# Kernel optimization log

Measured on AMD Instinct MI355X. Metric: run time of the kernel, lower is better.

Reference implementation:

```python
import jax, jax.numpy as jnp
import numpy as np

B, L, E, H, D = 32, 512, 256, 8, 64
SCALE = int(D ** 0.5)  # matches TF: int(hidden_dim ** 0.5) == 8


def setup_inputs() -> dict:
    key = jax.random.key(0)
    ks = jax.random.split(key, 6)
    return {
        "x": jax.random.normal(ks[0], (B, L, E), dtype=jnp.float32),
        "positional": jax.random.normal(ks[1], (L, E), dtype=jnp.float32) * 0.02,
        "Wq": jax.random.normal(ks[2], (H, E, D), dtype=jnp.float32) * 0.05,
        "Wk": jax.random.normal(ks[3], (H, E, D), dtype=jnp.float32) * 0.05,
        "Wv": jax.random.normal(ks[4], (H, E, D), dtype=jnp.float32) * 0.05,
        "Wo": jax.random.normal(ks[5], (H * D, E), dtype=jnp.float32) * 0.05,
    }


def reference(x, positional, Wq, Wk, Wv, Wo):
    act = jnp.tanh  # activation='tanh'
    xp = x + positional                                   # [B,L,E]
    # Batched per-head projections with activation applied post-matmul
    q = act(jnp.einsum('ble,hed->bhld', xp, Wq))          # [B,H,L,D]
    k = act(jnp.einsum('ble,hed->bhld', xp, Wk))
    v = act(jnp.einsum('ble,hed->bhld', xp, Wv))
    score = jnp.einsum('bhqd,bhkd->bhqk', q, k) / SCALE   # [B,H,L,L]
    attn = jax.nn.softmax(score, axis=-1)
    out = jnp.einsum('bhqk,bhkd->bhqd', attn, v)          # [B,H,L,D]
    # concat heads along last axis (head-major) -> [B,L,H*D]
    out = jnp.transpose(out, (0, 2, 1, 3)).reshape(B, L, H * D)
    return jnp.einsum('blf,fe->ble', out, Wo) + act(xp)   # [B,L,E]
```

## Files before the change

### kernel.cpp

```cpp
#include <hip/hip_runtime.h>
#include <cstdint>

#define NB 32
#define NL 512
#define NE 256
#define NH 8
#define ND 64
#define NM 16384
#define NHD 512

using half8  = __attribute__((ext_vector_type(8))) _Float16;
using half4  = __attribute__((ext_vector_type(4))) _Float16;
using f32x4  = __attribute__((ext_vector_type(4))) float;
using f32x16 = __attribute__((ext_vector_type(16))) float;
using u32x2  = __attribute__((ext_vector_type(2))) unsigned int;

__device__ __forceinline__ f32x4 mfma16(half8 a, half8 b, f32x4 c) {
    return __builtin_amdgcn_mfma_f32_16x16x32_f16(a, b, c, 0, 0, 0);
}
__device__ __forceinline__ f32x16 mfma32(half8 a, half8 b, f32x16 c) {
    return __builtin_amdgcn_mfma_f32_32x32x16_f16(a, b, c, 0, 0, 0);
}
__device__ __forceinline__ void cp16_g2l(const void* g, void* l) {
    __builtin_amdgcn_global_load_lds(
        (const __attribute__((address_space(1))) void*)g,
        (__attribute__((address_space(3))) void*)l, 16, 0, 0);
}
__device__ __forceinline__ float exp2fast(float x) {
    return __builtin_amdgcn_exp2f(x);
}
__device__ __forceinline__ float fast_tanh(float x) {
    float xc = fminf(fmaxf(x, -9.f), 9.f);
    float t = exp2fast(xc * 2.88539008178f);
    return (t - 1.f) * __builtin_amdgcn_rcpf(t + 1.f);
}
__device__ __forceinline__ uint32_t pk16(float a, float b) {
    auto h2 = __builtin_amdgcn_cvt_pkrtz(a, b);
    return __builtin_bit_cast(uint32_t, h2);
}

__global__ __launch_bounds__(256) void prep(
        const float* __restrict__ x, const float* __restrict__ pos,
        const float* __restrict__ Wq, const float* __restrict__ Wk,
        const float* __restrict__ Wv, const float* __restrict__ Wo,
        _Float16* __restrict__ wqkv, _Float16* __restrict__ woh,
        _Float16* __restrict__ xph) {
    int bid = blockIdx.x;
    if (bid < 2048) {
        int idx = bid * 256 + threadIdx.x;
        if (idx < 1536 * 256) {
            int n = idx >> 8, e = idx & 255;
            int s = n >> 9, h = (n >> 6) & 7, d = n & 63;
            const float* W = (s == 0) ? Wq : (s == 1) ? Wk : Wv;
            wqkv[idx] = (_Float16)W[(h * NE + e) * ND + d];
        } else {
            int j = idx - 1536 * 256;
            int e = j >> 9, f = j & 511;
            woh[j] = (_Float16)Wo[f * NE + e];
        }
    } else {
        int i = ((bid - 2048) * 256 + threadIdx.x) * 4;
        float4 xv = *(const float4*)(x + i);
        float4 pv = *(const float4*)(pos + (i & (NL * NE - 1)));
        half4 o;
        o[0] = (_Float16)(xv.x + pv.x);
        o[1] = (_Float16)(xv.y + pv.y);
        o[2] = (_Float16)(xv.z + pv.z);
        o[3] = (_Float16)(xv.w + pv.w);
        *(half4*)(xph + i) = o;
    }
}

__global__ __launch_bounds__(256) void proj_gemm(
        const _Float16* __restrict__ wqkv, const _Float16* __restrict__ xph,
        _Float16* __restrict__ q_all, _Float16* __restrict__ k_all,
        _Float16* __restrict__ vT) {
    __shared__ _Float16 Alds[128 * 64];
    __shared__ _Float16 Blds[128 * 64];
    int tid = threadIdx.x;
    int w = tid >> 6, l = tid & 63;
    int bid = blockIdx.x;
    int xcd = bid & 7, local = bid >> 3;
    int tn = local % 12;
    int tm = xcd * 16 + local / 12;
    int wn = w >> 1, wm = w & 1;
    int m16 = l & 15, g = l >> 4;
    bool isv = (tn >= 8);
    int lrow8 = l >> 3;
    int kc16 = (l & 7) ^ lrow8;
    f32x4 acc[4][4] = {};

    const _Float16* Ag = wqkv + (size_t)tn * 128 * 256;
    const _Float16* Bg = xph + (size_t)tm * 128 * 256;

    for (int kt = 0; kt < 4; ++kt) {
#pragma unroll
        for (int i = 0; i < 4; ++i) {
            int cA = w * 4 + i;
            int row = cA * 8 + lrow8;
            cp16_g2l(Ag + (size_t)row * 256 + kt * 64 + kc16 * 8,
                     Alds + cA * 512);
            cp16_g2l(Bg + (size_t)row * 256 + kt * 64 + kc16 * 8,
                     Blds + cA * 512);
        }
        __syncthreads();
#pragma unroll
        for (int ks = 0; ks < 2; ++ks) {
            half8 af[4], bf[4];
#pragma unroll
            for (int f = 0; f < 4; ++f) {
                int ra = wn * 64 + f * 16 + m16;
                int rb = wm * 64 + f * 16 + m16;
                af[f] = *(const half8*)(Alds + ra * 64 + (((ks * 4 + g) ^ (ra & 7)) << 3));
                bf[f] = *(const half8*)(Blds + rb * 64 + (((ks * 4 + g) ^ (rb & 7)) << 3));
            }
            if (!isv) {
#pragma unroll
                for (int nf = 0; nf < 4; ++nf)
#pragma unroll
                    for (int mf = 0; mf < 4; ++mf)
                        acc[nf][mf] = mfma16(af[nf], bf[mf], acc[nf][mf]);
            } else {
#pragma unroll
                for (int nf = 0; nf < 4; ++nf)
#pragma unroll
                    for (int mf = 0; mf < 4; ++mf)
                        acc[nf][mf] = mfma16(bf[mf], af[nf], acc[nf][mf]);
            }
        }
        __syncthreads();
    }
    if (!isv) {
        _Float16* dst = (tn < 4) ? q_all : k_all;
#pragma unroll
        for (int nf = 0; nf < 4; ++nf) {
            int c = (tn & 3) * 128 + wn * 64 + nf * 16 + g * 4;
#pragma unroll
            for (int mf = 0; mf < 4; ++mf) {
                int m = tm * 128 + wm * 64 + mf * 16 + m16;
                f32x4 v = acc[nf][mf];
                half4 hv;
#pragma unroll
                for (int r = 0; r < 4; ++r) hv[r] = (_Float16)fast_tanh(v[r]);
                *(half4*)(dst + (size_t)m * NHD + c) = hv;
            }
        }
    } else {
#pragma unroll
        for (int nf = 0; nf < 4; ++nf) {
            int c = (tn - 8) * 128 + wn * 64 + nf * 16 + m16;
#pragma unroll
            for (int mf = 0; mf < 4; ++mf) {
                int t0 = tm * 128 + wm * 64 + mf * 16 + g * 4;
                f32x4 v = acc[nf][mf];
                half4 hv;
#pragma unroll
                for (int r = 0; r < 4; ++r) hv[r] = (_Float16)fast_tanh(v[r]);
                *(half4*)(vT + (size_t)c * NM + t0) = hv;
            }
        }
    }
}

__global__ __launch_bounds__(256, 3) void attn_kernel(
        const _Float16* __restrict__ q_all, const _Float16* __restrict__ k_all,
        const _Float16* __restrict__ vT, _Float16* __restrict__ attn_out) {
    __shared__ _Float16 Klds[2][64 * 64];
    __shared__ _Float16 Vtlds[2][64 * 64];
    int tid = threadIdx.x;
    int w = tid >> 6, l = tid & 63;
    int l31 = l & 31, hi = l >> 5;
    int bid = blockIdx.x;
    int qt = bid & 3, h = (bid >> 2) & 7, b = bid >> 5;
    const float C1 = 0.125f * 1.44269504089f;

    int qbase = qt * 128 + w * 32;
    half8 qf[4];
    {
        const _Float16* qp = q_all + (size_t)(b * NL + qbase + l31) * NHD + h * ND + hi * 8;
#pragma unroll
        for (int ks = 0; ks < 4; ++ks) qf[ks] = *(const half8*)(qp + ks * 16);
    }

    f32x16 acc_o[2] = {};
    float mrow = -1e30f, lrow = 0.f;

    int st_row = tid >> 2;
    int st_u0 = (tid & 3) * 2;
    const _Float16* kg = k_all + (size_t)(b * NL + st_row) * NHD + h * ND + st_u0 * 8;
    const _Float16* vg = vT + (size_t)(h * ND + st_row) * NM + b * NL + st_u0 * 8;
    int so0 = st_row * 64 + ((st_u0 ^ (st_row & 7)) << 3);
    int so1 = st_row * 64 + (((st_u0 + 1) ^ (st_row & 7)) << 3);

    uint4 kv0 = *(const uint4*)(kg);
    uint4 kv1 = *(const uint4*)(kg + 8);
    uint4 vv0 = *(const uint4*)(vg);
    uint4 vv1 = *(const uint4*)(vg + 8);
    *(uint4*)&Klds[0][so0] = kv0;   *(uint4*)&Klds[0][so1] = kv1;
    *(uint4*)&Vtlds[0][so0] = vv0;  *(uint4*)&Vtlds[0][so1] = vv1;
    __syncthreads();

    for (int kt = 0; kt < 8; ++kt) {
        int cur = kt & 1;
        if (kt < 7) {
            const _Float16* kp = kg + (size_t)(kt + 1) * 64 * NHD;
            const _Float16* vp = vg + (kt + 1) * 64;
            kv0 = *(const uint4*)(kp);      kv1 = *(const uint4*)(kp + 8);
            vv0 = *(const uint4*)(vp);      vv1 = *(const uint4*)(vp + 8);
        }
        f32x16 acc_s[2] = {};
        __builtin_amdgcn_s_setprio(1);
#pragma unroll
        for (int ks = 0; ks < 4; ++ks)
#pragma unroll
            for (int kb2 = 0; kb2 < 2; ++kb2) {
                int key = kb2 * 32 + l31;
                half8 kb = *(const half8*)(&Klds[cur][key * 64 + (((ks * 2 + hi) ^ (key & 7)) << 3)]);
                acc_s[kb2] = mfma32(kb, qf[ks], acc_s[kb2]);
            }
        __builtin_amdgcn_s_setprio(0);
        float mx = -1e30f;
#pragma unroll
        for (int kb2 = 0; kb2 < 2; ++kb2)
#pragma unroll
            for (int j = 0; j < 16; ++j) mx = fmaxf(mx, acc_s[kb2][j]);
        mx = fmaxf(mx, __shfl_xor(mx, 32));
        mx *= 0.125f;
        if (!__all(mx <= mrow + 8.f)) {
            float mn = fmaxf(mrow, mx);
            float alpha = exp2fast((mrow - mn) * 1.44269504089f);
            mrow = mn;
            lrow *= alpha;
            float aq[16];
#pragma unroll
            for (int c = 0; c < 4; ++c)
#pragma unroll
                for (int r = 0; r < 4; ++r)
                    aq[c * 4 + r] = __shfl(alpha, c * 8 + hi * 4 + r);
#pragma unroll
            for (int d2 = 0; d2 < 2; ++d2)
#pragma unroll
                for (int j = 0; j < 16; ++j) acc_o[d2][j] *= aq[j];
        }
        float ml = mrow * 1.44269504089f;
        float rs = 0.f;
        uint32_t cw[2][4][2];
#pragma unroll
        for (int kb2 = 0; kb2 < 2; ++kb2)
#pragma unroll
            for (int a = 0; a < 4; ++a)
#pragma unroll
                for (int p = 0; p < 2; ++p) {
                    float p0 = exp2fast(fmaf(acc_s[kb2][4 * a + 2 * p],     C1, -ml));
                    float p1 = exp2fast(fmaf(acc_s[kb2][4 * a + 2 * p + 1], C1, -ml));
                    rs += p0 + p1;
                    cw[kb2][a][p] = pk16(p0, p1);
                }
        rs += __shfl_xor(rs, 32);
        lrow += rs;
        __builtin_amdgcn_s_setprio(1);
#pragma unroll
        for (int ks = 0; ks < 4; ++ks) {
            int kb2 = ks >> 1, s = ks & 1;
            u32x2 r0 = __builtin_amdgcn_permlane32_swap(
                cw[kb2][2 * s][0], cw[kb2][2 * s + 1][0], false, false);
            u32x2 r1 = __builtin_amdgcn_permlane32_swap(
                cw[kb2][2 * s][1], cw[kb2][2 * s + 1][1], false, false);
            union { uint32_t u[4]; half8 h; } pu;
            pu.u[0] = r0[0];  pu.u[1] = r1[0];
            pu.u[2] = r0[1];  pu.u[3] = r1[1];
#pragma unroll
            for (int d2 = 0; d2 < 2; ++d2) {
                int d = d2 * 32 + l31;
                half8 vb = *(const half8*)(&Vtlds[cur][d * 64 + (((ks * 2 + hi) ^ (d & 7)) << 3)]);
                acc_o[d2] = mfma32(pu.h, vb, acc_o[d2]);
            }
        }
        __builtin_amdgcn_s_setprio(0);
        if (kt < 7) {
            int nxt = cur ^ 1;
            *(uint4*)&Klds[nxt][so0] = kv0;   *(uint4*)&Klds[nxt][so1] = kv1;
            *(uint4*)&Vtlds[nxt][so0] = vv0;  *(uint4*)&Vtlds[nxt][so1] = vv1;
            __syncthreads();
        }
    }
    size_t orow0 = (size_t)(b * NL + qbase);
#pragma unroll
    for (int c = 0; c < 4; ++c)
#pragma unroll
        for (int r = 0; r < 4; ++r) {
            int qrow = c * 8 + hi * 4 + r;
            float inv = 1.f / __shfl(lrow, qrow);
#pragma unroll
            for (int d2 = 0; d2 < 2; ++d2)
                attn_out[(orow0 + qrow) * NHD + h * ND + d2 * 32 + l31] =
                    (_Float16)(acc_o[d2][c * 4 + r] * inv);
        }
}

__global__ __launch_bounds__(256) void final_gemm(
        const _Float16* __restrict__ woh, const _Float16* __restrict__ attn,
        const _Float16* __restrict__ xph, float* __restrict__ out) {
    __shared__ _Float16 Alds[2][128 * 64];
    __shared__ _Float16 Blds[2][64 * 64];
    int tid = threadIdx.x;
    int w = tid >> 6, l = tid & 63;
    int tn = blockIdx.x & 1, tm = blockIdx.x >> 1;
    int wn = w >> 1, wm = w & 1;
    int m16 = l & 15, g = l >> 4;
    int lrow8 = l >> 3;
    int kc16 = (l & 7) ^ lrow8;
    f32x4 acc[4][2] = {};

    const _Float16* Ag = woh + (size_t)tn * 128 * 512;
    const _Float16* Bg = attn + (size_t)tm * 64 * 512;

#define FIN_STAGE(kt, buf)                                                    \
    _Pragma("unroll") for (int i = 0; i < 4; ++i) {                           \
        int cA = w * 4 + i;                                                   \
        int row = cA * 8 + lrow8;                                             \
        cp16_g2l(Ag + (size_t)row * 512 + (kt) * 64 + kc16 * 8,               \
                 &Alds[buf][cA * 512]);                                       \
    }                                                                         \
    _Pragma("unroll") for (int i = 0; i < 2; ++i) {                           \
        int cB = w * 2 + i;                                                   \
        int row = cB * 8 + lrow8;                                             \
        cp16_g2l(Bg + (size_t)row * 512 + (kt) * 64 + kc16 * 8,               \
                 &Blds[buf][cB * 512]);                                       \
    }

    FIN_STAGE(0, 0);
    __syncthreads();
    int cur = 0;
    for (int kt = 0; kt < 8; ++kt) {
        if (kt < 7) { FIN_STAGE(kt + 1, cur ^ 1); }
#pragma unroll
        for (int ks = 0; ks < 2; ++ks) {
            half8 af[4], bf[2];
#pragma unroll
            for (int f = 0; f < 4; ++f) {
                int ra = wn * 64 + f * 16 + m16;
                af[f] = *(const half8*)(&Alds[cur][ra * 64 + (((ks * 4 + g) ^ (ra & 7)) << 3)]);
            }
#pragma unroll
            for (int f = 0; f < 2; ++f) {
                int rb = wm * 32 + f * 16 + m16;
                bf[f] = *(const half8*)(&Blds[cur][rb * 64 + (((ks * 4 + g) ^ (rb & 7)) << 3)]);
            }
#pragma unroll
            for (int nf = 0; nf < 4; ++nf)
#pragma unroll
                for (int mf = 0; mf < 2; ++mf)
                    acc[nf][mf] = mfma16(af[nf], bf[mf], acc[nf][mf]);
        }
        __syncthreads();
        cur ^= 1;
    }
#undef FIN_STAGE
#pragma unroll
    for (int nf = 0; nf < 4; ++nf) {
        int e = tn * 128 + wn * 64 + nf * 16 + g * 4;
#pragma unroll
        for (int mf = 0; mf < 2; ++mf) {
            int m = tm * 64 + wm * 32 + mf * 16 + m16;
            half4 hx = *(const half4*)(xph + (size_t)m * NE + e);
            f32x4 v = acc[nf][mf];
            float4 o;
            o.x = v[0] + fast_tanh((float)hx[0]);
            o.y = v[1] + fast_tanh((float)hx[1]);
            o.z = v[2] + fast_tanh((float)hx[2]);
            o.w = v[3] + fast_tanh((float)hx[3]);
            *(float4*)(out + (size_t)m * NE + e) = o;
        }
    }
}

extern "C" void kernel_launch(void* const* d_in, const int* in_sizes, int n_in,
                              void* d_out, int out_size, void* d_ws, size_t ws_size,
                              hipStream_t stream) {
    const float* x   = (const float*)d_in[0];
    const float* pos = (const float*)d_in[1];
    const float* Wq  = (const float*)d_in[2];
    const float* Wk  = (const float*)d_in[3];
    const float* Wv  = (const float*)d_in[4];
    const float* Wo  = (const float*)d_in[5];
    float* out = (float*)d_out;

    char* ws = (char*)d_ws;
    _Float16* xph   = (_Float16*)(ws);
    _Float16* wqkv  = (_Float16*)(ws + 8388608);
    _Float16* woh   = (_Float16*)(ws + 9175040);
    _Float16* q_all = (_Float16*)(ws + 9437184);
    _Float16* k_all = (_Float16*)(ws + 26214400);
    _Float16* vT    = (_Float16*)(ws + 42991616);
    _Float16* attn  = (_Float16*)(ws + 59768832);

    prep<<<dim3(6144), dim3(256), 0, stream>>>(x, pos, Wq, Wk, Wv, Wo, wqkv, woh, xph);
    proj_gemm<<<dim3(12 * 128), dim3(256), 0, stream>>>(wqkv, xph, q_all, k_all, vT);
    attn_kernel<<<dim3(1024), dim3(256), 0, stream>>>(q_all, k_all, vT, attn);
    final_gemm<<<dim3(512), dim3(256), 0, stream>>>(woh, attn, xph, out);
}
```

Before: 84.64 us.

## Fuse Q projection into attention kernel and remap blocks for XCD locality

The Q projection moves out of proj_gemm and into attn_kernel. Each attention block now computes its own 128x64 Q tile from xph and Wq using MFMA, applies tanh, and builds the register fragments with permlane32_swap. This removes the Q write and read round trip through global memory (16 MB). The cost is an extra GEMM prologue in every attention block, and the K/V LDS buffers are reused as scratch. Block-to-tile mapping is also changed in attn_kernel and final_gemm so that neighbouring tiles stay on the same XCD, improving L2 reuse.

```diff
diff --git a/kernel.cpp b/kernel.cpp
--- a/kernel.cpp
+++ b/kernel.cpp
@@ -73,24 +73,23 @@
 
 __global__ __launch_bounds__(256) void proj_gemm(
         const _Float16* __restrict__ wqkv, const _Float16* __restrict__ xph,
-        _Float16* __restrict__ q_all, _Float16* __restrict__ k_all,
-        _Float16* __restrict__ vT) {
+        _Float16* __restrict__ k_all, _Float16* __restrict__ vT) {
     __shared__ _Float16 Alds[128 * 64];
     __shared__ _Float16 Blds[128 * 64];
     int tid = threadIdx.x;
     int w = tid >> 6, l = tid & 63;
     int bid = blockIdx.x;
     int xcd = bid & 7, local = bid >> 3;
-    int tn = local % 12;
-    int tm = xcd * 16 + local / 12;
+    int tn = local & 7;
+    int tm = xcd * 16 + (local >> 3);
     int wn = w >> 1, wm = w & 1;
     int m16 = l & 15, g = l >> 4;
-    bool isv = (tn >= 8);
+    bool isv = (tn >= 4);
     int lrow8 = l >> 3;
     int kc16 = (l & 7) ^ lrow8;
     f32x4 acc[4][4] = {};
 
-    const _Float16* Ag = wqkv + (size_t)tn * 128 * 256;
+    const _Float16* Ag = wqkv + (size_t)(512 + tn * 128) * 256;
     const _Float16* Bg = xph + (size_t)tm * 128 * 256;
 
     for (int kt = 0; kt < 4; ++kt) {
@@ -131,10 +130,9 @@
         __syncthreads();
     }
     if (!isv) {
-        _Float16* dst = (tn < 4) ? q_all : k_all;
 #pragma unroll
         for (int nf = 0; nf < 4; ++nf) {
-            int c = (tn & 3) * 128 + wn * 64 + nf * 16 + g * 4;
+            int c = tn * 128 + wn * 64 + nf * 16 + g * 4;
 #pragma unroll
             for (int mf = 0; mf < 4; ++mf) {
                 int m = tm * 128 + wm * 64 + mf * 16 + m16;
@@ -142,13 +140,13 @@
                 half4 hv;
 #pragma unroll
                 for (int r = 0; r < 4; ++r) hv[r] = (_Float16)fast_tanh(v[r]);
-                *(half4*)(dst + (size_t)m * NHD + c) = hv;
+                *(half4*)(k_all + (size_t)m * NHD + c) = hv;
             }
         }
     } else {
 #pragma unroll
         for (int nf = 0; nf < 4; ++nf) {
-            int c = (tn - 8) * 128 + wn * 64 + nf * 16 + m16;
+            int c = (tn - 4) * 128 + wn * 64 + nf * 16 + m16;
 #pragma unroll
             for (int mf = 0; mf < 4; ++mf) {
                 int t0 = tm * 128 + wm * 64 + mf * 16 + g * 4;
@@ -163,23 +161,81 @@
 }
 
 __global__ __launch_bounds__(256, 3) void attn_kernel(
-        const _Float16* __restrict__ q_all, const _Float16* __restrict__ k_all,
-        const _Float16* __restrict__ vT, _Float16* __restrict__ attn_out) {
+        const _Float16* __restrict__ wqkv, const _Float16* __restrict__ xph,
+        const _Float16* __restrict__ k_all, const _Float16* __restrict__ vT,
+        _Float16* __restrict__ attn_out) {
     __shared__ _Float16 Klds[2][64 * 64];
     __shared__ _Float16 Vtlds[2][64 * 64];
     int tid = threadIdx.x;
     int w = tid >> 6, l = tid & 63;
     int l31 = l & 31, hi = l >> 5;
-    int bid = blockIdx.x;
-    int qt = bid & 3, h = (bid >> 2) & 7, b = bid >> 5;
+    int g0 = (blockIdx.x & 7) * 128 + (blockIdx.x >> 3);
+    int h = g0 & 7, bq = g0 >> 3;
+    int b = bq >> 2, qt = bq & 3;
     const float C1 = 0.125f * 1.44269504089f;
 
     int qbase = qt * 128 + w * 32;
+
+    _Float16* XQ = &Klds[0][0];
+    _Float16* WQ = &Vtlds[0][0];
+    f32x16 acc_q[2] = {};
+    {
+        const _Float16* xg = xph + (size_t)(b * NL + qt * 128) * 256;
+        const _Float16* wg = wqkv + (size_t)(h * 64) * 256;
+        int lrow8 = l >> 3;
+        int kc16 = (l & 7) ^ lrow8;
+        for (int kt = 0; kt < 4; ++kt) {
+#pragma unroll
+            for (int i = 0; i < 4; ++i) {
+                int c = w * 4 + i;
+                int row = c * 8 + lrow8;
+                cp16_g2l(xg + (size_t)row * 256 + kt * 64 + kc16 * 8, XQ + c * 512);
+            }
+#pragma unroll
+            for (int i = 0; i < 2; ++i) {
+                int c = w * 2 + i;
+                int row = c * 8 + lrow8;
+                cp16_g2l(wg + (size_t)row * 256 + kt * 64 + kc16 * 8, WQ + c * 512);
+            }
+            __syncthreads();
+#pragma unroll
+            for (int kp = 0; kp < 4; ++kp) {
+                int u = kp * 2 + hi;
+                int rq = w * 32 + l31;
+                half8 xf = *(const half8*)(XQ + rq * 64 + ((u ^ (rq & 7)) << 3));
+#pragma unroll
+                for (int d2 = 0; d2 < 2; ++d2) {
+                    int rd = d2 * 32 + l31;
+                    half8 wf = *(const half8*)(WQ + rd * 64 + ((u ^ (rd & 7)) << 3));
+                    acc_q[d2] = mfma32(wf, xf, acc_q[d2]);
+                }
+            }
+            __syncthreads();
+        }
+    }
     half8 qf[4];
     {
-        const _Float16* qp = q_all + (size_t)(b * NL + qbase + l31) * NHD + h * ND + hi * 8;
-#pragma unroll
-        for (int ks = 0; ks < 4; ++ks) qf[ks] = *(const half8*)(qp + ks * 16);
+        uint32_t qw[2][4][2];
+#pragma unroll
+        for (int d2 = 0; d2 < 2; ++d2)
+#pragma unroll
+            for (int a = 0; a < 4; ++a)
+#pragma unroll
+                for (int p = 0; p < 2; ++p)
+                    qw[d2][a][p] = pk16(fast_tanh(acc_q[d2][4 * a + 2 * p]),
+                                        fast_tanh(acc_q[d2][4 * a + 2 * p + 1]));
+#pragma unroll
+        for (int ks = 0; ks < 4; ++ks) {
+            int d2 = ks >> 1, s = ks & 1;
+            u32x2 r0 = __builtin_amdgcn_permlane32_swap(
+                qw[d2][2 * s][0], qw[d2][2 * s + 1][0], false, false);
+            u32x2 r1 = __builtin_amdgcn_permlane32_swap(
+                qw[d2][2 * s][1], qw[d2][2 * s + 1][1], false, false);
+            union { uint32_t u[4]; half8 h; } pu;
+            pu.u[0] = r0[0];  pu.u[1] = r1[0];
+            pu.u[2] = r0[1];  pu.u[3] = r1[1];
+            qf[ks] = pu.h;
+        }
     }
 
     f32x16 acc_o[2] = {};
@@ -305,7 +361,10 @@
     __shared__ _Float16 Blds[2][64 * 64];
     int tid = threadIdx.x;
     int w = tid >> 6, l = tid & 63;
-    int tn = blockIdx.x & 1, tm = blockIdx.x >> 1;
+    int bid = blockIdx.x;
+    int xcd = bid & 7, local = bid >> 3;
+    int tn = local & 1;
+    int tm = xcd * 32 + (local >> 1);
     int wn = w >> 1, wm = w & 1;
     int m16 = l & 15, g = l >> 4;
     int lrow8 = l >> 3;
@@ -390,13 +449,12 @@
     _Float16* xph   = (_Float16*)(ws);
     _Float16* wqkv  = (_Float16*)(ws + 8388608);
     _Float16* woh   = (_Float16*)(ws + 9175040);
-    _Float16* q_all = (_Float16*)(ws + 9437184);
-    _Float16* k_all = (_Float16*)(ws + 26214400);
-    _Float16* vT    = (_Float16*)(ws + 42991616);
-    _Float16* attn  = (_Float16*)(ws + 59768832);
+    _Float16* k_all = (_Float16*)(ws + 9437184);
+    _Float16* vT    = (_Float16*)(ws + 26214400);
+    _Float16* attn  = (_Float16*)(ws + 42991616);
 
     prep<<<dim3(6144), dim3(256), 0, stream>>>(x, pos, Wq, Wk, Wv, Wo, wqkv, woh, xph);
-    proj_gemm<<<dim3(12 * 128), dim3(256), 0, stream>>>(wqkv, xph, q_all, k_all, vT);
-    attn_kernel<<<dim3(1024), dim3(256), 0, stream>>>(q_all, k_all, vT, attn);
+    proj_gemm<<<dim3(1024), dim3(256), 0, stream>>>(wqkv, xph, k_all, vT);
+    attn_kernel<<<dim3(1024), dim3(256), 0, stream>>>(wqkv, xph, k_all, vT, attn);
     final_gemm<<<dim3(512), dim3(256), 0, stream>>>(woh, attn, xph, out);
 }
```

After: 78.52 us. -7.2%, faster.

## Fuse QKV projection into attention kernel, keeping K and V in LDS

Applied to the files above, without the earlier changes.

Merges the separate projection GEMM and the attention kernel into one 512-thread kernel per (batch, head). Each block computes Q, K and V for all 512 tokens, applies tanh, stages K and V^T for the whole sequence in LDS, then runs flash-style attention over them. This removes the global write and re-read of the Q/K/V intermediates and one kernel launch. The cost is only 256 blocks with 128 KB of LDS each, so fewer blocks fit per CU and latency hiding is weaker. The final GEMM's block index is also remapped to group tiles by XCD.

```diff
diff --git a/kernel.cpp b/kernel.cpp
--- a/kernel.cpp
+++ b/kernel.cpp
@@ -71,231 +71,214 @@
     }
 }
 
-__global__ __launch_bounds__(256) void proj_gemm(
+__global__ __launch_bounds__(512, 2) void attn_fused(
         const _Float16* __restrict__ wqkv, const _Float16* __restrict__ xph,
-        _Float16* __restrict__ q_all, _Float16* __restrict__ k_all,
-        _Float16* __restrict__ vT) {
-    __shared__ _Float16 Alds[128 * 64];
-    __shared__ _Float16 Blds[128 * 64];
+        _Float16* __restrict__ attn_out) {
+    __shared__ _Float16 Kp[512 * 64];
+    __shared__ _Float16 Vtp[64 * 512];
+    _Float16* Xs = Kp;
+    _Float16* Ws = Kp + 128 * 64;
+    _Float16* Qs = Vtp;
+
     int tid = threadIdx.x;
-    int w = tid >> 6, l = tid & 63;
-    int bid = blockIdx.x;
-    int xcd = bid & 7, local = bid >> 3;
-    int tn = local % 12;
-    int tm = xcd * 16 + local / 12;
-    int wn = w >> 1, wm = w & 1;
-    int m16 = l & 15, g = l >> 4;
-    bool isv = (tn >= 8);
+    int w8 = tid >> 6, l = tid & 63;
+    int l31 = l & 31, hi = l >> 5;
+    int rt = w8 & 3, d2w = w8 >> 2;
+    int g0 = ((blockIdx.x & 7) << 5) + (blockIdx.x >> 3);
+    int h = g0 & 7, b = g0 >> 3;
+    const float C1 = 0.125f * 1.44269504089f;
+
     int lrow8 = l >> 3;
     int kc16 = (l & 7) ^ lrow8;
-    f32x4 acc[4][4] = {};
-
-    const _Float16* Ag = wqkv + (size_t)tn * 128 * 256;
-    const _Float16* Bg = xph + (size_t)tm * 128 * 256;
-
-    for (int kt = 0; kt < 4; ++kt) {
-#pragma unroll
-        for (int i = 0; i < 4; ++i) {
-            int cA = w * 4 + i;
-            int row = cA * 8 + lrow8;
-            cp16_g2l(Ag + (size_t)row * 256 + kt * 64 + kc16 * 8,
-                     Alds + cA * 512);
-            cp16_g2l(Bg + (size_t)row * 256 + kt * 64 + kc16 * 8,
-                     Blds + cA * 512);
-        }
-        __syncthreads();
+    const _Float16* xg = xph + (size_t)(b * NL) * 256;
+    const _Float16* wg = wqkv + (size_t)(h * 64) * 256;
+
+    f32x16 acc_q[4] = {}, acc_k[4] = {}, acc_v[4] = {};
+    for (int kt2 = 0; kt2 < 4; ++kt2) {
+#pragma unroll
+        for (int r = 0; r < 4; ++r) {
+#pragma unroll
+            for (int i = 0; i < 2; ++i) {
+                int c = w8 * 2 + i;
+                int row = c * 8 + lrow8;
+                cp16_g2l(xg + (size_t)(r * 128 + row) * 256 + kt2 * 64 + kc16 * 8,
+                         Xs + c * 512);
+            }
+            if (r == 0) {
+                int row = w8 * 8 + lrow8;
+#pragma unroll
+                for (int s = 0; s < 3; ++s)
+                    cp16_g2l(wg + (size_t)s * 512 * 256 + (size_t)row * 256 + kt2 * 64 + kc16 * 8,
+                             Ws + s * 4096 + w8 * 512);
+            }
+            __syncthreads();
+#pragma unroll
+            for (int ks2 = 0; ks2 < 4; ++ks2) {
+                int rowb = rt * 32 + l31;
+                half8 bf = *(const half8*)(Xs + rowb * 64 + (((ks2 * 2 + hi) ^ (rowb & 7)) << 3));
+                int rowa = d2w * 32 + l31;
+                int sa = rowa * 64 + (((ks2 * 2 + hi) ^ (rowa & 7)) << 3);
+                half8 aq = *(const half8*)(Ws + sa);
+                half8 ak = *(const half8*)(Ws + 4096 + sa);
+                half8 av = *(const half8*)(Ws + 8192 + sa);
+                acc_q[r] = mfma32(aq, bf, acc_q[r]);
+                acc_k[r] = mfma32(ak, bf, acc_k[r]);
+                acc_v[r] = mfma32(bf, av, acc_v[r]);
+            }
+            __syncthreads();
+        }
+    }
+
+#pragma unroll
+    for (int r = 0; r < 4; ++r) {
+        uint32_t cq[4][2], ck[4][2];
+#pragma unroll
+        for (int a = 0; a < 4; ++a)
+#pragma unroll
+            for (int p = 0; p < 2; ++p) {
+                cq[a][p] = pk16(fast_tanh(acc_q[r][4 * a + 2 * p]),
+                                fast_tanh(acc_q[r][4 * a + 2 * p + 1]));
+                ck[a][p] = pk16(fast_tanh(acc_k[r][4 * a + 2 * p]),
+                                fast_tanh(acc_k[r][4 * a + 2 * p + 1]));
+            }
+        int rowq = r * 128 + rt * 32 + l31;
 #pragma unroll
         for (int ks = 0; ks < 2; ++ks) {
-            half8 af[4], bf[4];
-#pragma unroll
-            for (int f = 0; f < 4; ++f) {
-                int ra = wn * 64 + f * 16 + m16;
-                int rb = wm * 64 + f * 16 + m16;
-                af[f] = *(const half8*)(Alds + ra * 64 + (((ks * 4 + g) ^ (ra & 7)) << 3));
-                bf[f] = *(const half8*)(Blds + rb * 64 + (((ks * 4 + g) ^ (rb & 7)) << 3));
-            }
-            if (!isv) {
-#pragma unroll
-                for (int nf = 0; nf < 4; ++nf)
-#pragma unroll
-                    for (int mf = 0; mf < 4; ++mf)
-                        acc[nf][mf] = mfma16(af[nf], bf[mf], acc[nf][mf]);
-            } else {
-#pragma unroll
-                for (int nf = 0; nf < 4; ++nf)
-#pragma unroll
-                    for (int mf = 0; mf < 4; ++mf)
-                        acc[nf][mf] = mfma16(bf[mf], af[nf], acc[nf][mf]);
-            }
-        }
-        __syncthreads();
-    }
-    if (!isv) {
-        _Float16* dst = (tn < 4) ? q_all : k_all;
-#pragma unroll
-        for (int nf = 0; nf < 4; ++nf) {
-            int c = (tn & 3) * 128 + wn * 64 + nf * 16 + g * 4;
-#pragma unroll
-            for (int mf = 0; mf < 4; ++mf) {
-                int m = tm * 128 + wm * 64 + mf * 16 + m16;
-                f32x4 v = acc[nf][mf];
-                half4 hv;
-#pragma unroll
-                for (int r = 0; r < 4; ++r) hv[r] = (_Float16)fast_tanh(v[r]);
-                *(half4*)(dst + (size_t)m * NHD + c) = hv;
-            }
-        }
-    } else {
-#pragma unroll
-        for (int nf = 0; nf < 4; ++nf) {
-            int c = (tn - 8) * 128 + wn * 64 + nf * 16 + m16;
-#pragma unroll
-            for (int mf = 0; mf < 4; ++mf) {
-                int t0 = tm * 128 + wm * 64 + mf * 16 + g * 4;
-                f32x4 v = acc[nf][mf];
-                half4 hv;
-#pragma unroll
-                for (int r = 0; r < 4; ++r) hv[r] = (_Float16)fast_tanh(v[r]);
-                *(half4*)(vT + (size_t)c * NM + t0) = hv;
-            }
-        }
-    }
-}
-
-__global__ __launch_bounds__(256, 3) void attn_kernel(
-        const _Float16* __restrict__ q_all, const _Float16* __restrict__ k_all,
-        const _Float16* __restrict__ vT, _Float16* __restrict__ attn_out) {
-    __shared__ _Float16 Klds[2][64 * 64];
-    __shared__ _Float16 Vtlds[2][64 * 64];
-    int tid = threadIdx.x;
-    int w = tid >> 6, l = tid & 63;
-    int l31 = l & 31, hi = l >> 5;
-    int bid = blockIdx.x;
-    int qt = bid & 3, h = (bid >> 2) & 7, b = bid >> 5;
-    const float C1 = 0.125f * 1.44269504089f;
-
-    int qbase = qt * 128 + w * 32;
-    half8 qf[4];
-    {
-        const _Float16* qp = q_all + (size_t)(b * NL + qbase + l31) * NHD + h * ND + hi * 8;
-#pragma unroll
-        for (int ks = 0; ks < 4; ++ks) qf[ks] = *(const half8*)(qp + ks * 16);
-    }
-
-    f32x16 acc_o[2] = {};
-    float mrow = -1e30f, lrow = 0.f;
-
-    int st_row = tid >> 2;
-    int st_u0 = (tid & 3) * 2;
-    const _Float16* kg = k_all + (size_t)(b * NL + st_row) * NHD + h * ND + st_u0 * 8;
-    const _Float16* vg = vT + (size_t)(h * ND + st_row) * NM + b * NL + st_u0 * 8;
-    int so0 = st_row * 64 + ((st_u0 ^ (st_row & 7)) << 3);
-    int so1 = st_row * 64 + (((st_u0 + 1) ^ (st_row & 7)) << 3);
-
-    uint4 kv0 = *(const uint4*)(kg);
-    uint4 kv1 = *(const uint4*)(kg + 8);
-    uint4 vv0 = *(const uint4*)(vg);
-    uint4 vv1 = *(const uint4*)(vg + 8);
-    *(uint4*)&Klds[0][so0] = kv0;   *(uint4*)&Klds[0][so1] = kv1;
-    *(uint4*)&Vtlds[0][so0] = vv0;  *(uint4*)&Vtlds[0][so1] = vv1;
+            u32x2 q0 = __builtin_amdgcn_permlane32_swap(cq[2 * ks][0], cq[2 * ks + 1][0], false, false);
+            u32x2 q1 = __builtin_amdgcn_permlane32_swap(cq[2 * ks][1], cq[2 * ks + 1][1], false, false);
+            u32x2 k0 = __builtin_amdgcn_permlane32_swap(ck[2 * ks][0], ck[2 * ks + 1][0], false, false);
+            u32x2 k1 = __builtin_amdgcn_permlane32_swap(ck[2 * ks][1], ck[2 * ks + 1][1], false, false);
+            union { uint32_t u[4]; half8 h8; } pq, pk;
+            pq.u[0] = q0[0]; pq.u[1] = q1[0]; pq.u[2] = q0[1]; pq.u[3] = q1[1];
+            pk.u[0] = k0[0]; pk.u[1] = k1[0]; pk.u[2] = k0[1]; pk.u[3] = k1[1];
+            int uu = d2w * 4 + ks * 2 + hi;
+            *(half8*)(Qs + rowq * 64 + ((uu ^ (rowq & 7)) << 3)) = pq.h8;
+            *(half8*)(Kp + rowq * 64 + ((uu ^ (rowq & 7)) << 3)) = pk.h8;
+        }
+    }
     __syncthreads();
-
+    half8 qf[2][4];
+#pragma unroll
+    for (int qs = 0; qs < 2; ++qs)
+#pragma unroll
+        for (int ks = 0; ks < 4; ++ks) {
+            int q = w8 * 64 + qs * 32 + l31;
+            qf[qs][ks] = *(const half8*)(Qs + q * 64 + (((ks * 2 + hi) ^ (q & 7)) << 3));
+        }
+    __syncthreads();
+#pragma unroll
+    for (int r = 0; r < 4; ++r) {
+        uint32_t cv[4][2];
+#pragma unroll
+        for (int a = 0; a < 4; ++a)
+#pragma unroll
+            for (int p = 0; p < 2; ++p)
+                cv[a][p] = pk16(fast_tanh(acc_v[r][4 * a + 2 * p]),
+                                fast_tanh(acc_v[r][4 * a + 2 * p + 1]));
+        int d = d2w * 32 + l31;
+#pragma unroll
+        for (int ks = 0; ks < 2; ++ks) {
+            u32x2 v0 = __builtin_amdgcn_permlane32_swap(cv[2 * ks][0], cv[2 * ks + 1][0], false, false);
+            u32x2 v1 = __builtin_amdgcn_permlane32_swap(cv[2 * ks][1], cv[2 * ks + 1][1], false, false);
+            union { uint32_t u[4]; half8 h8; } pv;
+            pv.u[0] = v0[0]; pv.u[1] = v1[0]; pv.u[2] = v0[1]; pv.u[3] = v1[1];
+            int uu = r * 16 + rt * 4 + ks * 2 + hi;
+            *(half8*)(Vtp + d * 512 + ((uu ^ (d & 7)) << 3)) = pv.h8;
+        }
+    }
+    __syncthreads();
+
+    f32x16 acc_o[2][2] = {};
+    float mrow[2] = {-1e30f, -1e30f}, lrow[2] = {0.f, 0.f};
     for (int kt = 0; kt < 8; ++kt) {
-        int cur = kt & 1;
-        if (kt < 7) {
-            const _Float16* kp = kg + (size_t)(kt + 1) * 64 * NHD;
-            const _Float16* vp = vg + (kt + 1) * 64;
-            kv0 = *(const uint4*)(kp);      kv1 = *(const uint4*)(kp + 8);
-            vv0 = *(const uint4*)(vp);      vv1 = *(const uint4*)(vp + 8);
-        }
-        f32x16 acc_s[2] = {};
-        __builtin_amdgcn_s_setprio(1);
-#pragma unroll
-        for (int ks = 0; ks < 4; ++ks)
-#pragma unroll
-            for (int kb2 = 0; kb2 < 2; ++kb2) {
-                int key = kb2 * 32 + l31;
-                half8 kb = *(const half8*)(&Klds[cur][key * 64 + (((ks * 2 + hi) ^ (key & 7)) << 3)]);
-                acc_s[kb2] = mfma32(kb, qf[ks], acc_s[kb2]);
-            }
-        __builtin_amdgcn_s_setprio(0);
-        float mx = -1e30f;
-#pragma unroll
-        for (int kb2 = 0; kb2 < 2; ++kb2)
-#pragma unroll
-            for (int j = 0; j < 16; ++j) mx = fmaxf(mx, acc_s[kb2][j]);
-        mx = fmaxf(mx, __shfl_xor(mx, 32));
-        mx *= 0.125f;
-        if (!__all(mx <= mrow + 8.f)) {
-            float mn = fmaxf(mrow, mx);
-            float alpha = exp2fast((mrow - mn) * 1.44269504089f);
-            mrow = mn;
-            lrow *= alpha;
-            float aq[16];
-#pragma unroll
-            for (int c = 0; c < 4; ++c)
-#pragma unroll
-                for (int r = 0; r < 4; ++r)
-                    aq[c * 4 + r] = __shfl(alpha, c * 8 + hi * 4 + r);
-#pragma unroll
-            for (int d2 = 0; d2 < 2; ++d2)
-#pragma unroll
-                for (int j = 0; j < 16; ++j) acc_o[d2][j] *= aq[j];
-        }
-        float ml = mrow * 1.44269504089f;
-        float rs = 0.f;
-        uint32_t cw[2][4][2];
-#pragma unroll
-        for (int kb2 = 0; kb2 < 2; ++kb2)
-#pragma unroll
-            for (int a = 0; a < 4; ++a)
-#pragma unroll
-                for (int p = 0; p < 2; ++p) {
-                    float p0 = exp2fast(fmaf(acc_s[kb2][4 * a + 2 * p],     C1, -ml));
-                    float p1 = exp2fast(fmaf(acc_s[kb2][4 * a + 2 * p + 1], C1, -ml));
-                    rs += p0 + p1;
-                    cw[kb2][a][p] = pk16(p0, p1);
+#pragma unroll
+        for (int qs = 0; qs < 2; ++qs) {
+            f32x16 acc_s[2] = {};
+            __builtin_amdgcn_s_setprio(1);
+#pragma unroll
+            for (int ks = 0; ks < 4; ++ks)
+#pragma unroll
+                for (int kb2 = 0; kb2 < 2; ++kb2) {
+                    int key = kt * 64 + kb2 * 32 + l31;
+                    half8 kb = *(const half8*)(Kp + key * 64 + (((ks * 2 + hi) ^ (key & 7)) << 3));
+                    acc_s[kb2] = mfma32(kb, qf[qs][ks], acc_s[kb2]);
                 }
-        rs += __shfl_xor(rs, 32);
-        lrow += rs;
-        __builtin_amdgcn_s_setprio(1);
-#pragma unroll
-        for (int ks = 0; ks < 4; ++ks) {
-            int kb2 = ks >> 1, s = ks & 1;
-            u32x2 r0 = __builtin_amdgcn_permlane32_swap(
-                cw[kb2][2 * s][0], cw[kb2][2 * s + 1][0], false, false);
-            u32x2 r1 = __builtin_amdgcn_permlane32_swap(
-                cw[kb2][2 * s][1], cw[kb2][2 * s + 1][1], false, false);
-            union { uint32_t u[4]; half8 h; } pu;
-            pu.u[0] = r0[0];  pu.u[1] = r1[0];
-            pu.u[2] = r0[1];  pu.u[3] = r1[1];
-#pragma unroll
-            for (int d2 = 0; d2 < 2; ++d2) {
-                int d = d2 * 32 + l31;
-                half8 vb = *(const half8*)(&Vtlds[cur][d * 64 + (((ks * 2 + hi) ^ (d & 7)) << 3)]);
-                acc_o[d2] = mfma32(pu.h, vb, acc_o[d2]);
-            }
-        }
-        __builtin_amdgcn_s_setprio(0);
-        if (kt < 7) {
-            int nxt = cur ^ 1;
-            *(uint4*)&Klds[nxt][so0] = kv0;   *(uint4*)&Klds[nxt][so1] = kv1;
-            *(uint4*)&Vtlds[nxt][so0] = vv0;  *(uint4*)&Vtlds[nxt][so1] = vv1;
-            __syncthreads();
-        }
-    }
-    size_t orow0 = (size_t)(b * NL + qbase);
-#pragma unroll
-    for (int c = 0; c < 4; ++c)
-#pragma unroll
-        for (int r = 0; r < 4; ++r) {
-            int qrow = c * 8 + hi * 4 + r;
-            float inv = 1.f / __shfl(lrow, qrow);
-#pragma unroll
-            for (int d2 = 0; d2 < 2; ++d2)
-                attn_out[(orow0 + qrow) * NHD + h * ND + d2 * 32 + l31] =
-                    (_Float16)(acc_o[d2][c * 4 + r] * inv);
-        }
+            __builtin_amdgcn_s_setprio(0);
+            float mx = -1e30f;
+#pragma unroll
+            for (int kb2 = 0; kb2 < 2; ++kb2)
+#pragma unroll
+                for (int j = 0; j < 16; ++j) mx = fmaxf(mx, acc_s[kb2][j]);
+            mx = fmaxf(mx, __shfl_xor(mx, 32));
+            mx *= 0.125f;
+            if (!__all(mx <= mrow[qs] + 8.f)) {
+                float mn = fmaxf(mrow[qs], mx);
+                float alpha = exp2fast((mrow[qs] - mn) * 1.44269504089f);
+                mrow[qs] = mn;
+                lrow[qs] *= alpha;
+                float aq[16];
+#pragma unroll
+                for (int c = 0; c < 4; ++c)
+#pragma unroll
+                    for (int r = 0; r < 4; ++r)
+                        aq[c * 4 + r] = __shfl(alpha, c * 8 + hi * 4 + r);
+#pragma unroll
+                for (int d2 = 0; d2 < 2; ++d2)
+#pragma unroll
+                    for (int j = 0; j < 16; ++j) acc_o[qs][d2][j] *= aq[j];
+            }
+            float ml = mrow[qs] * 1.44269504089f;
+            float rs = 0.f;
+            uint32_t cw[2][4][2];
+#pragma unroll
+            for (int kb2 = 0; kb2 < 2; ++kb2)
+#pragma unroll
+                for (int a = 0; a < 4; ++a)
+#pragma unroll
+                    for (int p = 0; p < 2; ++p) {
+                        float p0 = exp2fast(fmaf(acc_s[kb2][4 * a + 2 * p],     C1, -ml));
+                        float p1 = exp2fast(fmaf(acc_s[kb2][4 * a + 2 * p + 1], C1, -ml));
+                        rs += p0 + p1;
+                        cw[kb2][a][p] = pk16(p0, p1);
+                    }
+            rs += __shfl_xor(rs, 32);
+            lrow[qs] += rs;
+            __builtin_amdgcn_s_setprio(1);
+#pragma unroll
+            for (int ks = 0; ks < 4; ++ks) {
+                int kb2 = ks >> 1, s = ks & 1;
+                u32x2 r0 = __builtin_amdgcn_permlane32_swap(
+                    cw[kb2][2 * s][0], cw[kb2][2 * s + 1][0], false, false);
+                u32x2 r1 = __builtin_amdgcn_permlane32_swap(
+                    cw[kb2][2 * s][1], cw[kb2][2 * s + 1][1], false, false);
+                union { uint32_t u[4]; half8 h8; } pu;
+                pu.u[0] = r0[0]; pu.u[1] = r1[0]; pu.u[2] = r0[1]; pu.u[3] = r1[1];
+#pragma unroll
+                for (int d2 = 0; d2 < 2; ++d2) {
+                    int d = d2 * 32 + l31;
+                    int uu = kt * 8 + ks * 2 + hi;
+                    half8 vb = *(const half8*)(Vtp + d * 512 + ((uu ^ (d & 7)) << 3));
+                    acc_o[qs][d2] = mfma32(pu.h8, vb, acc_o[qs][d2]);
+                }
+            }
+            __builtin_amdgcn_s_setprio(0);
+        }
+    }
+#pragma unroll
+    for (int qs = 0; qs < 2; ++qs) {
+        size_t orow0 = (size_t)(b * NL + w8 * 64 + qs * 32);
+#pragma unroll
+        for (int c = 0; c < 4; ++c)
+#pragma unroll
+            for (int r = 0; r < 4; ++r) {
+                int qrow = c * 8 + hi * 4 + r;
+                float inv = 1.f / __shfl(lrow[qs], qrow);
+#pragma unroll
+                for (int d2 = 0; d2 < 2; ++d2)
+                    attn_out[(orow0 + qrow) * NHD + h * ND + d2 * 32 + l31] =
+                        (_Float16)(acc_o[qs][d2][c * 4 + r] * inv);
+            }
+    }
 }
 
 __global__ __launch_bounds__(256) void final_gemm(
@@ -305,7 +288,10 @@
     __shared__ _Float16 Blds[2][64 * 64];
     int tid = threadIdx.x;
     int w = tid >> 6, l = tid & 63;
-    int tn = blockIdx.x & 1, tm = blockIdx.x >> 1;
+    int bid = blockIdx.x;
+    int xcd = bid & 7, local = bid >> 3;
+    int tn = local & 1;
+    int tm = xcd * 32 + (local >> 1);
     int wn = w >> 1, wm = w & 1;
     int m16 = l & 15, g = l >> 4;
     int lrow8 = l >> 3;
@@ -390,13 +376,9 @@
     _Float16* xph   = (_Float16*)(ws);
     _Float16* wqkv  = (_Float16*)(ws + 8388608);
     _Float16* woh   = (_Float16*)(ws + 9175040);
-    _Float16* q_all = (_Float16*)(ws + 9437184);
-    _Float16* k_all = (_Float16*)(ws + 26214400);
-    _Float16* vT    = (_Float16*)(ws + 42991616);
-    _Float16* attn  = (_Float16*)(ws + 59768832);
+    _Float16* attn  = (_Float16*)(ws + 9437184);
 
     prep<<<dim3(6144), dim3(256), 0, stream>>>(x, pos, Wq, Wk, Wv, Wo, wqkv, woh, xph);
-    proj_gemm<<<dim3(12 * 128), dim3(256), 0, stream>>>(wqkv, xph, q_all, k_all, vT);
-    attn_kernel<<<dim3(1024), dim3(256), 0, stream>>>(q_all, k_all, vT, attn);
+    attn_fused<<<dim3(256), dim3(512), 0, stream>>>(wqkv, xph, attn);
     final_gemm<<<dim3(512), dim3(256), 0, stream>>>(woh, attn, xph, out);
 }
```

After: 74.33 us. 12.2% less time.
